# Performance work log

Measured on AMD Instinct MI355X. Metric: run time of the kernel, lower is better.

Reference implementation:

```python
import jax, jax.numpy as jnp
import numpy as np

N_NODES = 100_000
N_EDGES = 1_000_000
N_GRAPHS = 2048
F_IN, N_HEADS, HEAD_DIM = 128, 2, 32
NEG_SLOPE = 0.2


def seg_softmax(logits, seg, num):
    # numerically stable scatter-softmax over segments (leading axis)
    m = jax.ops.segment_max(logits, seg, num_segments=num)
    e = jnp.exp(logits - m[seg])
    s = jax.ops.segment_sum(e, seg, num_segments=num)
    return e / s[seg]


def setup_inputs() -> dict:
    key = jax.random.key(0)
    ks = jax.random.split(key, 10)
    HC = N_HEADS * HEAD_DIM
    x = jax.random.normal(ks[0], (N_NODES, F_IN), jnp.float32)
    edge_index = jax.random.randint(ks[1], (2, N_EDGES), 0, N_NODES, jnp.int32)
    batch = jnp.sort(jax.random.randint(ks[2], (N_NODES,), 0, N_GRAPHS, jnp.int32))
    sc_in = 1.0 / np.sqrt(F_IN)
    sc_hc = 1.0 / np.sqrt(HC)
    W_l = jax.random.normal(ks[3], (F_IN, HC), jnp.float32) * sc_in
    W_r = jax.random.normal(ks[4], (F_IN, HC), jnp.float32) * sc_in
    att = jax.random.normal(ks[5], (N_HEADS, HEAD_DIM), jnp.float32) * (1.0 / np.sqrt(HEAD_DIM))
    bias = jnp.zeros((HC,), jnp.float32)
    w_rel = jax.random.normal(ks[6], (HC,), jnp.float32) * sc_hc
    w_root = jax.random.normal(ks[7], (HC,), jnp.float32) * sc_hc
    b_score = jnp.zeros((1,), jnp.float32)
    return {"x": x, "edge_index": edge_index, "batch": batch, "W_l": W_l,
            "W_r": W_r, "att": att, "bias": bias, "w_rel": w_rel,
            "w_root": w_root, "b_score": b_score}


def reference(x, edge_index, batch, W_l, W_r, att, bias, w_rel, w_root, b_score):
    N = x.shape[0]
    H, C = att.shape
    src, dst = edge_index[0], edge_index[1]
    # --- GATv2Conv (add_self_loops=True, concat heads, negative_slope=0.2) ---
    loop = jnp.arange(N, dtype=src.dtype)
    s = jnp.concatenate([src, loop])  # source j
    d = jnp.concatenate([dst, loop])  # target i
    xl = (x @ W_l).reshape(N, H, C)   # lin_l -> source features
    xr = (x @ W_r).reshape(N, H, C)   # lin_r -> target features
    e = jax.nn.leaky_relu(xl[s] + xr[d], NEG_SLOPE)       # [E', H, C]
    logits = jnp.einsum('ehc,hc->eh', e, att)              # [E', H]
    alpha = seg_softmax(logits, d, N)                      # softmax over incoming edges per target
    h = jax.ops.segment_sum(xl[s] * alpha[:, :, None], d, num_segments=N)
    h = h.reshape(N, H * C) + bias                         # conv output (data.x)
    # --- SAGPooling(min_score=-1): softmax(GraphConv score) keeps all nodes ---
    aggr = jax.ops.segment_sum(h[src], dst, num_segments=N)  # GraphConv neighbor add-aggr
    score = aggr @ w_rel + h @ w_root + b_score              # [N]
    sm = seg_softmax(score, batch, N_GRAPHS)
    px = h * sm[:, None]
    # --- global_add_pool + global_mean_pool ---
    add = jax.ops.segment_sum(px, batch, num_segments=N_GRAPHS)
    cnt = jax.ops.segment_sum(jnp.ones((N,), px.dtype), batch, num_segments=N_GRAPHS)
    mean = add / jnp.maximum(cnt, 1.0)[:, None]
    return add + mean  # global_emb [N_GRAPHS, H*C]
```

## Files before the change

### kernel.cpp

```cpp
#include <hip/hip_runtime.h>
#include <hip/hip_bf16.h>

#define N_NODES 100000
#define N_EDGES 1000000
#define N_GRAPHS 2048
#define F_IN 128
#define NEG_SLOPE 0.2f
#define E_TOT (N_EDGES + N_NODES)
#define SCAN_BLK 98
#define GEMM_BLOCKS 782
#define HIST_BLOCKS ((E_TOT + 255) / 256)
#define NODE_BLOCKS ((N_NODES + 255) / 256)

template <int CTRL>
__device__ __forceinline__ float dpp_add(float x) {
    return x + __int_as_float(__builtin_amdgcn_update_dpp(
        0, __float_as_int(x), CTRL, 0xf, 0xf, true));
}
__device__ __forceinline__ float head_sum_bcast(float x) {
    x = dpp_add<0x111>(x);
    x = dpp_add<0x112>(x);
    x = dpp_add<0x114>(x);
    x = dpp_add<0x118>(x);
    x = dpp_add<0x142>(x);
    return __int_as_float(__builtin_amdgcn_ds_swizzle(__float_as_int(x), 0x03E0));
}
__device__ __forceinline__ float full_sum64(float x) {
    x = dpp_add<0x111>(x);
    x = dpp_add<0x112>(x);
    x = dpp_add<0x114>(x);
    x = dpp_add<0x118>(x);
    x = dpp_add<0x142>(x);
    x = dpp_add<0x143>(x);
    return x;
}

__global__ __launch_bounds__(256) void k_gemm_hist(const float* __restrict__ x,
                                                   const float* __restrict__ Wl,
                                                   const float* __restrict__ Wr,
                                                   const int* __restrict__ ei,
                                                   float* __restrict__ xlr,
                                                   int* __restrict__ counts,
                                                   int* __restrict__ rank_) {
    if (blockIdx.x >= GEMM_BLOCKS) {
        int e = (blockIdx.x - GEMM_BLOCKS) * 256 + threadIdx.x;
        if (e < E_TOT) {
            int d = (e < N_EDGES) ? ei[N_EDGES + e] : (e - N_EDGES);
            rank_[e] = atomicAdd(&counts[d], 1);
        }
        return;
    }
    __shared__ float xT[8][132];
    __shared__ float wsm[8][132];
    int tid = threadIdx.x;
    int row0 = blockIdx.x * 128;
    int tx = tid & 15, ty = tid >> 4;
    int sr = tid >> 1;
    int sk = (tid & 1) * 4;
    int wk = tid >> 5;
    int wc = (tid & 31) * 4;
    float acc[8][8];
#pragma unroll
    for (int i = 0; i < 8; ++i)
#pragma unroll
        for (int j = 0; j < 8; ++j) acc[i][j] = 0.f;

    for (int k0 = 0; k0 < F_IN; k0 += 8) {
        int r = row0 + sr;
        float4 xv = (r < N_NODES) ? *(const float4*)(x + (size_t)r * F_IN + k0 + sk)
                                  : make_float4(0.f, 0.f, 0.f, 0.f);
        xT[sk + 0][sr] = xv.x; xT[sk + 1][sr] = xv.y;
        xT[sk + 2][sr] = xv.z; xT[sk + 3][sr] = xv.w;
        float4 wv = (wc < 64) ? *(const float4*)(Wl + (size_t)(k0 + wk) * 64 + wc)
                              : *(const float4*)(Wr + (size_t)(k0 + wk) * 64 + wc - 64);
        *(float4*)&wsm[wk][wc] = wv;
        __syncthreads();
#pragma unroll
        for (int kk = 0; kk < 8; ++kk) {
            float a[8], b[8];
            *(float4*)&a[0] = *(float4*)&xT[kk][ty * 8];
            *(float4*)&a[4] = *(float4*)&xT[kk][ty * 8 + 4];
            *(float4*)&b[0] = *(float4*)&wsm[kk][tx * 8];
            *(float4*)&b[4] = *(float4*)&wsm[kk][tx * 8 + 4];
#pragma unroll
            for (int i = 0; i < 8; ++i)
#pragma unroll
                for (int j = 0; j < 8; ++j) acc[i][j] += a[i] * b[j];
        }
        __syncthreads();
    }
#pragma unroll
    for (int i = 0; i < 8; ++i) {
        int r = row0 + ty * 8 + i;
        if (r < N_NODES) {
            *(float4*)(xlr + (size_t)r * 128 + tx * 8)     = make_float4(acc[i][0], acc[i][1], acc[i][2], acc[i][3]);
            *(float4*)(xlr + (size_t)r * 128 + tx * 8 + 4) = make_float4(acc[i][4], acc[i][5], acc[i][6], acc[i][7]);
        }
    }
}

__global__ __launch_bounds__(256) void k_scanA(const int* __restrict__ counts,
                                               int* __restrict__ rowptr,
                                               int* __restrict__ bsum) {
    __shared__ int sh[256];
    int t = threadIdx.x, b = blockIdx.x;
    int base = b * 1024 + t * 4;
    int v[4]; int s = 0;
#pragma unroll
    for (int i = 0; i < 4; ++i) {
        int idx = base + i;
        v[i] = (idx < N_NODES) ? counts[idx] : 0;
        s += v[i];
    }
    sh[t] = s; __syncthreads();
    for (int off = 1; off < 256; off <<= 1) {
        int xv = (t >= off) ? sh[t - off] : 0;
        __syncthreads();
        sh[t] += xv;
        __syncthreads();
    }
    int run = sh[t] - s;
    if (t == 255) bsum[b] = sh[255];
#pragma unroll
    for (int i = 0; i < 4; ++i) {
        int idx = base + i;
        if (idx < N_NODES) rowptr[idx] = run;
        run += v[i];
    }
}

__global__ __launch_bounds__(256) void k_scanC_bounds(int* __restrict__ rowptr,
                                                      const int* __restrict__ bsum,
                                                      const int* __restrict__ batch,
                                                      int* __restrict__ start) {
    if (blockIdx.x < NODE_BLOCKS) {
        int i = blockIdx.x * 256 + threadIdx.x;
        int target = blockIdx.x >> 2;
        int lane = threadIdx.x & 63;
        int p = 0;
        if (lane < target)                    p  = bsum[lane];
        if (lane + 64 < target && lane + 64 < SCAN_BLK) p += bsum[lane + 64];
#pragma unroll
        for (int o = 1; o < 64; o <<= 1) p += __shfl_xor(p, o, 64);
        if (i < N_NODES) rowptr[i] += p;
        if (blockIdx.x == 0 && threadIdx.x == 0) rowptr[N_NODES] = E_TOT;
    } else {
        int i = (blockIdx.x - NODE_BLOCKS) * 256 + threadIdx.x;
        if (i >= N_NODES) return;
        int bi = batch[i];
        int bp = (i == 0) ? -1 : batch[i - 1];
        for (int g = bp + 1; g <= bi; ++g) start[g] = i;
        if (i == N_NODES - 1)
            for (int g = bi + 1; g <= N_GRAPHS; ++g) start[g] = N_NODES;
    }
}

__global__ __launch_bounds__(256) void k_scatter(const int* __restrict__ ei,
                                                 const int* __restrict__ rowptr,
                                                 const int* __restrict__ rank_,
                                                 int* __restrict__ sorted_src) {
    int e = blockIdx.x * 256 + threadIdx.x;
    if (e >= E_TOT) return;
    int s, d;
    if (e < N_EDGES) { s = ei[e]; d = ei[N_EDGES + e]; }
    else             { s = d = e - N_EDGES; }
    sorted_src[rowptr[d] + rank_[e]] = s;
}

__global__ __launch_bounds__(256) void k_gat(const float* __restrict__ xlr,
                                             const int* __restrict__ rowptr,
                                             const int* __restrict__ sorted_src,
                                             const float* __restrict__ att,
                                             const float* __restrict__ bias,
                                             const float* __restrict__ w_rel,
                                             const float* __restrict__ w_root,
                                             float* __restrict__ hfeat,
                                             float* __restrict__ tbuf,
                                             float* __restrict__ rbuf) {
    int lane = threadIdx.x & 63;
    int du = __builtin_amdgcn_readfirstlane(blockIdx.x * 4 + (threadIdx.x >> 6));
    if (du >= N_NODES) return;
    float xr_l  = xlr[(size_t)du * 128 + 64 + lane];
    float att_l = att[lane];
    int j0 = __builtin_amdgcn_readfirstlane(rowptr[du]);
    int j1 = __builtin_amdgcn_readfirstlane(rowptr[du + 1]);
    float m = -1e30f, wsum = 0.f, acc = 0.f;
    for (int jc = j0; jc < j1; jc += 8) {
        int n = j1 - jc;
        int jj = jc + (lane & 7);
        if (jj > j1 - 1) jj = j1 - 1;
        int sv = sorted_src[jj];
        float p[8], xv[8];
#pragma unroll
        for (int i = 0; i < 8; ++i) {
            int s = __builtin_amdgcn_readlane(sv, i);
            const float* ps = xlr + (size_t)(unsigned)s * 128;
            xv[i] = ps[lane];
        }
#pragma unroll
        for (int i = 0; i < 8; ++i) {
            float v = xv[i] + xr_l;
            v = (v > 0.f) ? v : NEG_SLOPE * v;
            p[i] = v * att_l;
        }
#pragma unroll
        for (int i = 0; i < 8; ++i)
            p[i] = head_sum_bcast(p[i]);
#pragma unroll
        for (int i = 0; i < 8; ++i)
            if (i >= n) p[i] = -1e30f;
        float mc = p[0];
#pragma unroll
        for (int i = 1; i < 8; ++i) mc = fmaxf(mc, p[i]);
        float cws = 0.f, cacc = 0.f;
#pragma unroll
        for (int i = 0; i < 8; ++i) {
            float w = __expf(p[i] - mc);
            cws += w;
            cacc += w * xv[i];
        }
        float mnew = fmaxf(m, mc);
        float fo = __expf(m - mnew), fn = __expf(mc - mnew);
        wsum = wsum * fo + cws * fn;
        acc  = acc  * fo + cacc * fn;
        m = mnew;
    }
    float h = acc / wsum + bias[lane];
    hfeat[(size_t)du * 64 + lane] = h;
    float a = full_sum64(h * w_rel[lane]);
    float b = full_sum64(h * w_root[lane]);
    if (lane == 63) { tbuf[du] = a; rbuf[du] = b; }
}

__global__ __launch_bounds__(256) void k_pool(const int* __restrict__ rowptr,
                                              const int* __restrict__ sorted_src,
                                              const float* __restrict__ t,
                                              const float* __restrict__ r,
                                              const float* __restrict__ b_score,
                                              float* __restrict__ score,
                                              const float* __restrict__ h,
                                              const int* __restrict__ start,
                                              float* __restrict__ out) {
    __shared__ float sh[4];
    __shared__ float shacc[4][64];
    int g = blockIdx.x;
    int tid = threadIdx.x, w = tid >> 6, lane = tid & 63;
    int n0 = start[g], n1 = start[g + 1];
    int cnt = n1 - n0;
    if (cnt <= 0) { if (tid < 64) out[(size_t)g * 64 + tid] = 0.f; return; }
    float bsc = b_score[0];
    for (int i = n0 + tid; i < n1; i += 256) {
        int jj0 = rowptr[i], jj1 = rowptr[i + 1];
        float sum = 0.f;
        int j = jj0;
        for (; j + 4 <= jj1; j += 4) {
            int s0 = sorted_src[j], s1 = sorted_src[j + 1];
            int s2 = sorted_src[j + 2], s3 = sorted_src[j + 3];
            sum += t[s0] + t[s1] + t[s2] + t[s3];
        }
        for (; j < jj1; ++j) sum += t[sorted_src[j]];
        score[i] = sum - t[i] + r[i] + bsc;
    }
    __syncthreads();
    float m = -1e30f;
    for (int i = n0 + tid; i < n1; i += 256) m = fmaxf(m, score[i]);
#pragma unroll
    for (int o = 32; o; o >>= 1) m = fmaxf(m, __shfl_xor(m, o, 64));
    if (lane == 0) sh[w] = m;
    __syncthreads();
    m = fmaxf(fmaxf(sh[0], sh[1]), fmaxf(sh[2], sh[3]));
    float ssum = 0.f;
    for (int i = n0 + tid; i < n1; i += 256) ssum += __expf(score[i] - m);
#pragma unroll
    for (int o = 32; o; o >>= 1) ssum += __shfl_xor(ssum, o, 64);
    __syncthreads();
    if (lane == 0) sh[w] = ssum;
    __syncthreads();
    ssum = sh[0] + sh[1] + sh[2] + sh[3];
    float acc = 0.f;
    for (int i = n0 + w; i < n1; i += 4)
        acc += __expf(score[i] - m) * h[(size_t)i * 64 + lane];
    shacc[w][lane] = acc;
    __syncthreads();
    if (w == 0) {
        float tot = shacc[0][lane] + shacc[1][lane] + shacc[2][lane] + shacc[3][lane];
        out[(size_t)g * 64 + lane] = tot * (1.f + 1.f / (float)cnt) / ssum;
    }
}

extern "C" void kernel_launch(void* const* d_in, const int* in_sizes, int n_in,
                              void* d_out, int out_size, void* d_ws, size_t ws_size,
                              hipStream_t stream) {
    const float* x      = (const float*)d_in[0];
    const int*   ei     = (const int*)d_in[1];
    const int*   batch  = (const int*)d_in[2];
    const float* Wl     = (const float*)d_in[3];
    const float* Wr     = (const float*)d_in[4];
    const float* att    = (const float*)d_in[5];
    const float* bias   = (const float*)d_in[6];
    const float* w_rel  = (const float*)d_in[7];
    const float* w_root = (const float*)d_in[8];
    const float* b_sc   = (const float*)d_in[9];

    char* ws = (char*)d_ws;
    size_t off = 0;
    auto alloc = [&](size_t bytes) { void* p = ws + off; off += (bytes + 255) & ~255ull; return p; };
    float* xlr        = (float*)alloc((size_t)N_NODES * 128 * 4);
    float* hfeat      = (float*)alloc((size_t)N_NODES * 64 * 4);
    int*   sorted_src = (int*)  alloc((size_t)E_TOT * 4);
    int*   rank_      = (int*)  alloc((size_t)E_TOT * 4);
    int*   counts     = (int*)  alloc((size_t)N_NODES * 4);
    int*   rowptr     = (int*)  alloc((size_t)(N_NODES + 1) * 4);
    int*   bsum       = (int*)  alloc((size_t)SCAN_BLK * 4);
    float* tbuf       = (float*)alloc((size_t)N_NODES * 4);
    float* rbuf       = (float*)alloc((size_t)N_NODES * 4);
    float* score      = (float*)alloc((size_t)N_NODES * 4);
    int*   start      = (int*)  alloc((size_t)(N_GRAPHS + 1) * 4);

    (void)hipMemsetAsync(counts, 0, (size_t)N_NODES * 4, stream);

    k_gemm_hist   <<<GEMM_BLOCKS + HIST_BLOCKS, 256, 0, stream>>>(x, Wl, Wr, ei, xlr, counts, rank_);
    k_scanA       <<<SCAN_BLK, 256, 0, stream>>>(counts, rowptr, bsum);
    k_scanC_bounds<<<NODE_BLOCKS * 2, 256, 0, stream>>>(rowptr, bsum, batch, start);
    k_scatter     <<<(E_TOT + 255) / 256, 256, 0, stream>>>(ei, rowptr, rank_, sorted_src);
    k_gat         <<<(N_NODES + 3) / 4, 256, 0, stream>>>(xlr, rowptr, sorted_src, att, bias,
                                                          w_rel, w_root, hfeat, tbuf, rbuf);
    k_pool        <<<N_GRAPHS, 256, 0, stream>>>(rowptr, sorted_src, tbuf, rbuf, b_sc,
                                                 score, hfeat, start, (float*)d_out);
}
```

Before: 265.3 us.

## Compute node projection GEMM with split-bf16 MFMA instead of FP32 FMA

Replaces the scalar FP32 register-tiled GEMM for x@[W_l|W_r] with 32x32x16 bf16 MFMA instructions. Inputs and weights are split into hi/lo bf16 parts and three MFMAs per tile recover near-FP32 accuracy. Weights are staged transposed in LDS as bf16 pairs, and x is read straight from global memory per lane. The aim is to cut GEMM compute time, at the cost of extra conversion work, strided scalar output stores and slightly reduced precision.

Result: faster. 249.0 us (-6.1%).

```diff
diff --git a/kernel.cpp b/kernel.cpp
--- a/kernel.cpp
+++ b/kernel.cpp
@@ -11,6 +11,18 @@
 #define GEMM_BLOCKS 782
 #define HIST_BLOCKS ((E_TOT + 255) / 256)
 #define NODE_BLOCKS ((N_NODES + 255) / 256)
+
+typedef short  bf16x8 __attribute__((ext_vector_type(8)));
+typedef float  f32x16 __attribute__((ext_vector_type(16)));
+
+__device__ __forceinline__ short f2bf(float f) {
+    unsigned u = __float_as_uint(f);
+    unsigned r = (u + 0x7fffu + ((u >> 16) & 1u)) >> 16;
+    return (short)r;
+}
+__device__ __forceinline__ float bf2f(short h) {
+    return __uint_as_float(((unsigned)(unsigned short)h) << 16);
+}
 
 template <int CTRL>
 __device__ __forceinline__ float dpp_add(float x) {
@@ -50,53 +62,72 @@
         }
         return;
     }
-    __shared__ float xT[8][132];
-    __shared__ float wsm[8][132];
+    __shared__ short wt[2][128][136];
     int tid = threadIdx.x;
-    int row0 = blockIdx.x * 128;
-    int tx = tid & 15, ty = tid >> 4;
-    int sr = tid >> 1;
-    int sk = (tid & 1) * 4;
-    int wk = tid >> 5;
-    int wc = (tid & 31) * 4;
-    float acc[8][8];
-#pragma unroll
-    for (int i = 0; i < 8; ++i)
-#pragma unroll
-        for (int j = 0; j < 8; ++j) acc[i][j] = 0.f;
-
-    for (int k0 = 0; k0 < F_IN; k0 += 8) {
-        int r = row0 + sr;
-        float4 xv = (r < N_NODES) ? *(const float4*)(x + (size_t)r * F_IN + k0 + sk)
-                                  : make_float4(0.f, 0.f, 0.f, 0.f);
-        xT[sk + 0][sr] = xv.x; xT[sk + 1][sr] = xv.y;
-        xT[sk + 2][sr] = xv.z; xT[sk + 3][sr] = xv.w;
-        float4 wv = (wc < 64) ? *(const float4*)(Wl + (size_t)(k0 + wk) * 64 + wc)
-                              : *(const float4*)(Wr + (size_t)(k0 + wk) * 64 + wc - 64);
-        *(float4*)&wsm[wk][wc] = wv;
-        __syncthreads();
-#pragma unroll
-        for (int kk = 0; kk < 8; ++kk) {
-            float a[8], b[8];
-            *(float4*)&a[0] = *(float4*)&xT[kk][ty * 8];
-            *(float4*)&a[4] = *(float4*)&xT[kk][ty * 8 + 4];
-            *(float4*)&b[0] = *(float4*)&wsm[kk][tx * 8];
-            *(float4*)&b[4] = *(float4*)&wsm[kk][tx * 8 + 4];
-#pragma unroll
-            for (int i = 0; i < 8; ++i)
-#pragma unroll
-                for (int j = 0; j < 8; ++j) acc[i][j] += a[i] * b[j];
-        }
-        __syncthreads();
-    }
-#pragma unroll
-    for (int i = 0; i < 8; ++i) {
-        int r = row0 + ty * 8 + i;
-        if (r < N_NODES) {
-            *(float4*)(xlr + (size_t)r * 128 + tx * 8)     = make_float4(acc[i][0], acc[i][1], acc[i][2], acc[i][3]);
-            *(float4*)(xlr + (size_t)r * 128 + tx * 8 + 4) = make_float4(acc[i][4], acc[i][5], acc[i][6], acc[i][7]);
-        }
-    }
+    {
+        int k  = tid >> 1;
+        int cq = tid & 1;
+        const float* Wsrc = cq ? Wr : Wl;
+#pragma unroll
+        for (int u = 0; u < 16; ++u) {
+            int c0 = u * 4;
+            float4 wv = *(const float4*)(Wsrc + (size_t)k * 64 + c0);
+            float vv[4] = {wv.x, wv.y, wv.z, wv.w};
+#pragma unroll
+            for (int q = 0; q < 4; ++q) {
+                int c = cq * 64 + c0 + q;
+                short hi = f2bf(vv[q]);
+                wt[0][c][k] = hi;
+                wt[1][c][k] = f2bf(vv[q] - bf2f(hi));
+            }
+        }
+    }
+    __syncthreads();
+    int lane = tid & 63, w = tid >> 6;
+    int m = lane & 31, half = lane >> 5;
+    int row = blockIdx.x * 128 + w * 32 + m;
+    bool rv = row < N_NODES;
+    const float* xrow = x + (size_t)(rv ? row : 0) * F_IN;
+    f32x16 acc[4];
+#pragma unroll
+    for (int t = 0; t < 4; ++t)
+#pragma unroll
+        for (int i = 0; i < 16; ++i) acc[t][i] = 0.f;
+
+#pragma unroll
+    for (int kt = 0; kt < 8; ++kt) {
+        int kb = kt * 16 + half * 8;
+        float4 xa = rv ? *(const float4*)(xrow + kb)
+                       : make_float4(0.f, 0.f, 0.f, 0.f);
+        float4 xb = rv ? *(const float4*)(xrow + kb + 4)
+                       : make_float4(0.f, 0.f, 0.f, 0.f);
+        float xs[8] = {xa.x, xa.y, xa.z, xa.w, xb.x, xb.y, xb.z, xb.w};
+        bf16x8 ahi, alo;
+#pragma unroll
+        for (int j = 0; j < 8; ++j) {
+            short hi = f2bf(xs[j]);
+            ahi[j] = hi;
+            alo[j] = f2bf(xs[j] - bf2f(hi));
+        }
+#pragma unroll
+        for (int t = 0; t < 4; ++t) {
+            int n = t * 32 + m;
+            bf16x8 bhi = *(const bf16x8*)&wt[0][n][kb];
+            bf16x8 blo = *(const bf16x8*)&wt[1][n][kb];
+            acc[t] = __builtin_amdgcn_mfma_f32_32x32x16_bf16(ahi, bhi, acc[t], 0, 0, 0);
+            acc[t] = __builtin_amdgcn_mfma_f32_32x32x16_bf16(ahi, blo, acc[t], 0, 0, 0);
+            acc[t] = __builtin_amdgcn_mfma_f32_32x32x16_bf16(alo, bhi, acc[t], 0, 0, 0);
+        }
+    }
+    int r0 = blockIdx.x * 128 + w * 32 + 4 * half;
+#pragma unroll
+    for (int t = 0; t < 4; ++t)
+#pragma unroll
+        for (int reg = 0; reg < 16; ++reg) {
+            int rr = r0 + (reg & 3) + 8 * (reg >> 2);
+            if (rr < N_NODES)
+                xlr[(size_t)rr * 128 + t * 32 + m] = acc[t][reg];
+        }
 }
 
 __global__ __launch_bounds__(256) void k_scanA(const int* __restrict__ counts,
@@ -215,9 +246,9 @@
         float cws = 0.f, cacc = 0.f;
 #pragma unroll
         for (int i = 0; i < 8; ++i) {
-            float w = __expf(p[i] - mc);
-            cws += w;
-            cacc += w * xv[i];
+            float wgt = __expf(p[i] - mc);
+            cws += wgt;
+            cacc += wgt * xv[i];
         }
         float mnew = fmaxf(m, mc);
         float fo = __expf(m - mnew), fn = __expf(mc - mnew);
```
